# Kernel tuning notes

Hardware: AMD Instinct MI355X
Metric: run time of the kernel (lower is better)

The kernel has to match this reference:

```python
import jax, jax.numpy as jnp
import numpy as np

IN_CH = 8        # input_channels (includes time channel)
HID = 64         # hidden_channels
OUT = 1          # output_channels
MLP_W = 128      # CDEFunc hidden width
B, T = 4096, 166


def setup_inputs() -> dict:
    key = jax.random.key(0)
    ks = jax.random.split(key, 12)
    s = lambda fan_in: 1.0 / np.sqrt(fan_in)
    u0 = jax.random.normal(ks[0], (B, IN_CH - 1), dtype=jnp.float32)
    coeffs = jax.random.normal(ks[1], (B, T, IN_CH), dtype=jnp.float32)
    # CDEFunc params
    W1 = jax.random.uniform(ks[2], (HID, MLP_W), jnp.float32, -s(HID), s(HID))
    b1 = jax.random.uniform(ks[3], (MLP_W,), jnp.float32, -s(HID), s(HID))
    W2 = jax.random.uniform(ks[4], (MLP_W, IN_CH * HID), jnp.float32, -s(MLP_W), s(MLP_W))
    b2 = jax.random.uniform(ks[5], (IN_CH * HID,), jnp.float32, -s(MLP_W), s(MLP_W))
    # initial / readout linears
    Wi = jax.random.uniform(ks[6], (IN_CH - 1, HID), jnp.float32, -s(IN_CH - 1), s(IN_CH - 1))
    bi = jax.random.uniform(ks[7], (HID,), jnp.float32, -s(IN_CH - 1), s(IN_CH - 1))
    Wr = jax.random.uniform(ks[8], (HID, OUT), jnp.float32, -s(HID), s(HID))
    br = jax.random.uniform(ks[9], (OUT,), jnp.float32, -s(HID), s(HID))
    return {"u0": u0, "coeffs": coeffs, "W1": W1, "b1": b1, "W2": W2,
            "b2": b2, "Wi": Wi, "bi": bi, "Wr": Wr, "br": br}


def _cde_forward(u0, coeffs, W1, b1, W2, b2, Wi, bi, Wr, br):
    z0 = u0 @ Wi + bi                                  # [B, HID]
    # Linear interpolation on the knot grid t=0..T-1 with Euler steps of dt=1:
    # z_{k+1} = z_k + f(z_k) @ (X_{k+1} - X_k)
    dX = coeffs[:, 1:] - coeffs[:, :-1]                # [B, T-1, IN_CH]
    dX_t = jnp.swapaxes(dX, 0, 1)                      # [T-1, B, IN_CH]

    def step(z, dx):
        h = jax.nn.relu(z @ W1 + b1)                   # [B, MLP_W]
        f = jnp.tanh(h @ W2 + b2)                      # [B, IN_CH*HID]
        f = f.reshape(z.shape[0], HID, IN_CH)          # [B, HID, IN_CH]
        z_new = z + jnp.einsum('bhi,bi->bh', f, dx)
        return z_new, z_new

    _, zs = jax.lax.scan(step, z0, dX_t)               # [T-1, B, HID]
    z_all = jnp.concatenate([z0[None], zs], axis=0)    # [T, B, HID]
    z_all = jnp.swapaxes(z_all, 0, 1)                  # [B, T, HID]
    return z_all @ Wr + br                             # [B, T, OUT]


def reference(u0, coeffs, W1, b1, W2, b2, Wi, bi, Wr, br):
    return _cde_forward(u0, coeffs, W1, b1, W2, b2, Wi, bi, Wr, br)
```

## Files before the change

### kernel.cpp

```cpp
#include <hip/hip_runtime.h>


#define NBLK 256
#define NT   512
#define RB   16
#define T_LEN 166
#define IC   8
#define HID  64
#define MW   128
#define NF   512
#define ZSTR 65
#define DXSTR 12

typedef _Float16 half8 __attribute__((ext_vector_type(8)));
typedef _Float16 half4 __attribute__((ext_vector_type(4)));
typedef float    f32x4 __attribute__((ext_vector_type(4)));

__device__ __forceinline__ float fast_tanh(float x) {
    float e = __expf(2.0f * x);
    return 1.0f - 2.0f * __builtin_amdgcn_rcpf(e + 1.0f);
}

__global__ __launch_bounds__(NT, 2)
void cde_fused(const float* __restrict__ u0, const float* __restrict__ coeffs,
               const float* __restrict__ W1, const float* __restrict__ b1,
               const float* __restrict__ W2, const float* __restrict__ b2,
               const float* __restrict__ Wi, const float* __restrict__ bi,
               const float* __restrict__ Wr, const float* __restrict__ br,
               float* __restrict__ out)
{
    __shared__ __align__(16) unsigned char hh[RB * 256];
    __shared__ __align__(16) unsigned char hl[RB * 256];
    __shared__ __align__(16) unsigned char zh[RB * 128];
    __shared__ __align__(16) unsigned char zl[RB * 128];
    __shared__ float zbuf[RB * ZSTR];
    __shared__ __align__(16) float dxp[RB * DXSTR];

    const int tid  = threadIdx.x;
    const int lane = tid & 63;
    const int w    = tid >> 6;
    const int l15  = lane & 15;
    const int lq   = lane >> 4;
    const int swzr = (l15 & 7) << 4;
    const int b0   = blockIdx.x * RB;

    half8 w1h[2], w1l[2];
    #pragma unroll
    for (int kt = 0; kt < 2; ++kt) {
        const int krow = kt * 32 + lq * 8;
        const int ncol = w * 16 + l15;
        half8 vh, vl;
        #pragma unroll
        for (int j = 0; j < 8; ++j) {
            const float x = W1[(krow + j) * MW + ncol];
            const _Float16 hi = (_Float16)x;
            vh[j] = hi; vl[j] = (_Float16)(x - (float)hi);
        }
        w1h[kt] = vh; w1l[kt] = vl;
    }
    half8 w2h[16], w2l[16];
    #pragma unroll
    for (int q = 0; q < 4; ++q) {
        #pragma unroll
        for (int kt = 0; kt < 4; ++kt) {
            const int krow = kt * 32 + lq * 8;
            const int ncol = (w * 4 + q) * 16 + l15;
            half8 vh, vl;
            #pragma unroll
            for (int j = 0; j < 8; ++j) {
                const float x = W2[(krow + j) * NF + ncol];
                const _Float16 hi = (_Float16)x;
                vh[j] = hi; vl[j] = (_Float16)(x - (float)hi);
            }
            w2h[q * 4 + kt] = vh; w2l[q * 4 + kt] = vl;
        }
    }
    const f32x4 b1v = *(const f32x4*)(b1 + w * 16 + lq * 4);
    f32x4 b2v[4];
    #pragma unroll
    for (int q = 0; q < 4; ++q)
        b2v[q] = *(const f32x4*)(b2 + (w * 4 + q) * 16 + lq * 4);

    float wr0 = 0.f, wr1 = 0.f, wr2 = 0.f, wr3 = 0.f;
    const float brv = br[0];
    if (tid < 256) {
        const int seg = tid & 15;
        wr0 = Wr[seg * 4 + 0]; wr1 = Wr[seg * 4 + 1];
        wr2 = Wr[seg * 4 + 2]; wr3 = Wr[seg * 4 + 3];
    }

    #pragma unroll
    for (int s = 0; s < 2; ++s) {
        const int o = tid + NT * s;
        const int r = o >> 6, k = o & 63;
        float acc = bi[k];
        #pragma unroll
        for (int c = 0; c < 7; ++c) acc += u0[(b0 + r) * 7 + c] * Wi[c * HID + k];
        zbuf[r * ZSTR + k] = acc;
        const int byte = r * 128 + ((k * 2) ^ ((r & 7) << 4));
        const _Float16 hi = (_Float16)acc;
        *(_Float16*)(zh + byte) = hi;
        *(_Float16*)(zl + byte) = (_Float16)(acc - (float)hi);
    }
    __syncthreads();

    for (int t = 0; t < T_LEN; ++t) {
        if (tid < 256) {
            const int r = tid >> 4, seg = tid & 15;
            const float* zr = zbuf + r * ZSTR + seg * 4;
            float p = zr[0] * wr0 + zr[1] * wr1 + zr[2] * wr2 + zr[3] * wr3;
            p += __shfl_xor(p, 1, 64);
            p += __shfl_xor(p, 2, 64);
            p += __shfl_xor(p, 4, 64);
            p += __shfl_xor(p, 8, 64);
            if (seg == 0) out[(size_t)(b0 + r) * T_LEN + t] = p + brv;
        }
        if (t == T_LEN - 1) break;

        if (tid < 128) {
            const int r = tid >> 3, i = tid & 7;
            const float* cp = coeffs + ((size_t)(b0 + r) * T_LEN + t) * IC + i;
            dxp[r * DXSTR + i] = cp[IC] - cp[0];
        }

        f32x4 acc1 = {0.f, 0.f, 0.f, 0.f};
        #pragma unroll
        for (int kt = 0; kt < 2; ++kt) {
            const int off = l15 * 128 + ((kt * 64 + lq * 16) ^ swzr);
            const half8 zfh = *(const half8*)(zh + off);
            const half8 zfl = *(const half8*)(zl + off);
            acc1 = __builtin_amdgcn_mfma_f32_16x16x32_f16(w1h[kt], zfh, acc1, 0, 0, 0);
            acc1 = __builtin_amdgcn_mfma_f32_16x16x32_f16(w1l[kt], zfh, acc1, 0, 0, 0);
            acc1 = __builtin_amdgcn_mfma_f32_16x16x32_f16(w1h[kt], zfl, acc1, 0, 0, 0);
        }
        half4 ph, pl;
        #pragma unroll
        for (int r = 0; r < 4; ++r) {
            const float hv = fmaxf(acc1[r] + b1v[r], 0.0f);
            const _Float16 hi = (_Float16)hv;
            ph[r] = hi; pl[r] = (_Float16)(hv - (float)hi);
        }
        const int hoff = l15 * 256 + ((w * 32 + lq * 8) ^ swzr);
        *(half4*)(hh + hoff) = ph;
        *(half4*)(hl + hoff) = pl;
        __syncthreads();

        half8 bhf[4], blf[4];
        #pragma unroll
        for (int kt = 0; kt < 4; ++kt) {
            const int off = l15 * 256 + ((kt * 64 + lq * 16) ^ swzr);
            bhf[kt] = *(const half8*)(hh + off);
            blf[kt] = *(const half8*)(hl + off);
        }
        const f32x4 dxv = *(const f32x4*)(dxp + l15 * DXSTR + (lq & 1) * 4);
        #pragma unroll
        for (int q = 0; q < 4; ++q) {
            f32x4 acc = {0.f, 0.f, 0.f, 0.f};
            #pragma unroll
            for (int kt = 0; kt < 4; ++kt) {
                acc = __builtin_amdgcn_mfma_f32_16x16x32_f16(w2h[q * 4 + kt], bhf[kt], acc, 0, 0, 0);
                acc = __builtin_amdgcn_mfma_f32_16x16x32_f16(w2l[q * 4 + kt], bhf[kt], acc, 0, 0, 0);
                acc = __builtin_amdgcn_mfma_f32_16x16x32_f16(w2h[q * 4 + kt], blf[kt], acc, 0, 0, 0);
            }
            float s = 0.f;
            #pragma unroll
            for (int r = 0; r < 4; ++r) {
                const float f = fast_tanh(acc[r] + b2v[q][r]);
                s = fmaf(f, dxv[r], s);
            }
            s += __shfl_xor(s, 16, 64);
            if ((lq & 1) == 0) {
                const int kh = (w * 4 + q) * 2 + (lq >> 1);
                const float zn = zbuf[l15 * ZSTR + kh] + s;
                zbuf[l15 * ZSTR + kh] = zn;
                const _Float16 hi = (_Float16)zn;
                const int zoff = l15 * 128 + ((kh * 2) ^ swzr);
                *(_Float16*)(zh + zoff) = hi;
                *(_Float16*)(zl + zoff) = (_Float16)(zn - (float)hi);
            }
        }
        __syncthreads();
    }
}

extern "C" void kernel_launch(void* const* d_in, const int* in_sizes, int n_in,
                              void* d_out, int out_size, void* d_ws, size_t ws_size,
                              hipStream_t stream) {
    const float* u0     = (const float*)d_in[0];
    const float* coeffs = (const float*)d_in[1];
    const float* W1     = (const float*)d_in[2];
    const float* b1     = (const float*)d_in[3];
    const float* W2     = (const float*)d_in[4];
    const float* b2     = (const float*)d_in[5];
    const float* Wi     = (const float*)d_in[6];
    const float* bi     = (const float*)d_in[7];
    const float* Wr     = (const float*)d_in[8];
    const float* br     = (const float*)d_in[9];
    cde_fused<<<NBLK, NT, 0, stream>>>(u0, coeffs, W1, b1, W2, b2, Wi, bi, Wr, br,
                                       (float*)d_out);
}
```

Before: 320.2 us.

## Keep hidden state in registers, prefetch coeffs, use lgkm-only barriers

The fp32 hidden state now lives in per-wave registers (z8) instead of a shared zbuf, and updates use cross-lane shuffles. dX is computed in registers from a coefficient row prefetched one step ahead, so the per-step shared dxp staging is gone. The readout becomes per-wave partial dot products reduced by one wave, and __syncthreads is replaced by an LDS-only waitcnt plus s_barrier. Together these are meant to cut LDS traffic, global-load latency on the critical path and barrier cost in the serial time loop. The catch is that barrier correctness now depends on the inline asm waitcnt, and there is some extra register pressure.

```diff
diff --git a/kernel.cpp b/kernel.cpp
--- a/kernel.cpp
+++ b/kernel.cpp
@@ -5,12 +5,11 @@
 #define NT   512
 #define RB   16
 #define T_LEN 166
+#define NSTEP 165
 #define IC   8
 #define HID  64
 #define MW   128
 #define NF   512
-#define ZSTR 65
-#define DXSTR 12
 
 typedef _Float16 half8 __attribute__((ext_vector_type(8)));
 typedef _Float16 half4 __attribute__((ext_vector_type(4)));
@@ -19,6 +18,12 @@
 __device__ __forceinline__ float fast_tanh(float x) {
     float e = __expf(2.0f * x);
     return 1.0f - 2.0f * __builtin_amdgcn_rcpf(e + 1.0f);
+}
+
+__device__ __forceinline__ void bar_lgkm() {
+    asm volatile("s_waitcnt lgkmcnt(0)" ::: "memory");
+    __builtin_amdgcn_s_barrier();
+    __builtin_amdgcn_sched_barrier(0);
 }
 
 __global__ __launch_bounds__(NT, 2)
@@ -33,8 +38,7 @@
     __shared__ __align__(16) unsigned char hl[RB * 256];
     __shared__ __align__(16) unsigned char zh[RB * 128];
     __shared__ __align__(16) unsigned char zl[RB * 128];
-    __shared__ float zbuf[RB * ZSTR];
-    __shared__ __align__(16) float dxp[RB * DXSTR];
+    __shared__ float part[8][17];
 
     const int tid  = threadIdx.x;
     const int lane = tid & 63;
@@ -81,46 +85,54 @@
     for (int q = 0; q < 4; ++q)
         b2v[q] = *(const f32x4*)(b2 + (w * 4 + q) * 16 + lq * 4);
 
-    float wr0 = 0.f, wr1 = 0.f, wr2 = 0.f, wr3 = 0.f;
+    float wrs[8];
+    #pragma unroll
+    for (int j = 0; j < 8; ++j) wrs[j] = Wr[w * 8 + j];
     const float brv = br[0];
-    if (tid < 256) {
-        const int seg = tid & 15;
-        wr0 = Wr[seg * 4 + 0]; wr1 = Wr[seg * 4 + 1];
-        wr2 = Wr[seg * 4 + 2]; wr3 = Wr[seg * 4 + 3];
-    }
-
-    #pragma unroll
-    for (int s = 0; s < 2; ++s) {
-        const int o = tid + NT * s;
-        const int r = o >> 6, k = o & 63;
-        float acc = bi[k];
-        #pragma unroll
-        for (int c = 0; c < 7; ++c) acc += u0[(b0 + r) * 7 + c] * Wi[c * HID + k];
-        zbuf[r * ZSTR + k] = acc;
-        const int byte = r * 128 + ((k * 2) ^ ((r & 7) << 4));
-        const _Float16 hi = (_Float16)acc;
-        *(_Float16*)(zh + byte) = hi;
-        *(_Float16*)(zl + byte) = (_Float16)(acc - (float)hi);
-    }
+
+    float z8[8];
+    {
+        float uu[7];
+        const float* ur = u0 + (size_t)(b0 + l15) * 7;
+        #pragma unroll
+        for (int c = 0; c < 7; ++c) uu[c] = ur[c];
+        #pragma unroll
+        for (int j = 0; j < 8; ++j) {
+            float a = bi[w * 8 + j];
+            #pragma unroll
+            for (int c = 0; c < 7; ++c) a = fmaf(uu[c], Wi[c * HID + w * 8 + j], a);
+            z8[j] = a;
+        }
+    }
+    {
+        half8 hi8, lo8;
+        #pragma unroll
+        for (int j = 0; j < 8; ++j) {
+            const _Float16 hi = (_Float16)z8[j];
+            hi8[j] = hi; lo8[j] = (_Float16)(z8[j] - (float)hi);
+        }
+        if (lq == 0) {
+            const int zoff = l15 * 128 + ((w * 16) ^ swzr);
+            *(half8*)(zh + zoff) = hi8;
+            *(half8*)(zl + zoff) = lo8;
+            float rp = 0.f;
+            #pragma unroll
+            for (int j = 0; j < 8; ++j) rp = fmaf(z8[j], wrs[j], rp);
+            part[w][l15] = rp;
+        }
+    }
+    const float* cbase = coeffs + (size_t)(b0 + l15) * T_LEN * IC + (lq & 1) * 4;
+    f32x4 ccur = *(const f32x4*)(cbase);
     __syncthreads();
 
-    for (int t = 0; t < T_LEN; ++t) {
-        if (tid < 256) {
-            const int r = tid >> 4, seg = tid & 15;
-            const float* zr = zbuf + r * ZSTR + seg * 4;
-            float p = zr[0] * wr0 + zr[1] * wr1 + zr[2] * wr2 + zr[3] * wr3;
-            p += __shfl_xor(p, 1, 64);
-            p += __shfl_xor(p, 2, 64);
-            p += __shfl_xor(p, 4, 64);
-            p += __shfl_xor(p, 8, 64);
-            if (seg == 0) out[(size_t)(b0 + r) * T_LEN + t] = p + brv;
-        }
-        if (t == T_LEN - 1) break;
-
-        if (tid < 128) {
-            const int r = tid >> 3, i = tid & 7;
-            const float* cp = coeffs + ((size_t)(b0 + r) * T_LEN + t) * IC + i;
-            dxp[r * DXSTR + i] = cp[IC] - cp[0];
+    for (int t = 0; t < NSTEP; ++t) {
+        const f32x4 cnext = *(const f32x4*)(cbase + (size_t)(t + 1) * IC);
+
+        if (w == 7) {
+            float v = part[lq][l15] + part[lq + 4][l15];
+            v += __shfl_xor(v, 16, 64);
+            v += __shfl_xor(v, 32, 64);
+            if (lq == 0) out[(size_t)(b0 + l15) * T_LEN + t] = v + brv;
         }
 
         f32x4 acc1 = {0.f, 0.f, 0.f, 0.f};
@@ -143,7 +155,7 @@
         const int hoff = l15 * 256 + ((w * 32 + lq * 8) ^ swzr);
         *(half4*)(hh + hoff) = ph;
         *(half4*)(hl + hoff) = pl;
-        __syncthreads();
+        bar_lgkm();
 
         half8 bhf[4], blf[4];
         #pragma unroll
@@ -152,7 +164,7 @@
             bhf[kt] = *(const half8*)(hh + off);
             blf[kt] = *(const half8*)(hl + off);
         }
-        const f32x4 dxv = *(const f32x4*)(dxp + l15 * DXSTR + (lq & 1) * 4);
+        const f32x4 dxv = cnext - ccur;
         #pragma unroll
         for (int q = 0; q < 4; ++q) {
             f32x4 acc = {0.f, 0.f, 0.f, 0.f};
@@ -164,22 +176,39 @@
             }
             float s = 0.f;
             #pragma unroll
-            for (int r = 0; r < 4; ++r) {
-                const float f = fast_tanh(acc[r] + b2v[q][r]);
-                s = fmaf(f, dxv[r], s);
-            }
-            s += __shfl_xor(s, 16, 64);
-            if ((lq & 1) == 0) {
-                const int kh = (w * 4 + q) * 2 + (lq >> 1);
-                const float zn = zbuf[l15 * ZSTR + kh] + s;
-                zbuf[l15 * ZSTR + kh] = zn;
-                const _Float16 hi = (_Float16)zn;
-                const int zoff = l15 * 128 + ((kh * 2) ^ swzr);
-                *(_Float16*)(zh + zoff) = hi;
-                *(_Float16*)(zl + zoff) = (_Float16)(zn - (float)hi);
-            }
-        }
-        __syncthreads();
+            for (int r = 0; r < 4; ++r)
+                s = fmaf(fast_tanh(acc[r] + b2v[q][r]), dxv[r], s);
+            const float tt = s + __shfl_xor(s, 16, 64);
+            const float uu = __shfl_xor(tt, 32, 64);
+            z8[2 * q]     += tt;
+            z8[2 * q + 1] += uu;
+        }
+        {
+            half8 hi8, lo8;
+            #pragma unroll
+            for (int j = 0; j < 8; ++j) {
+                const _Float16 hi = (_Float16)z8[j];
+                hi8[j] = hi; lo8[j] = (_Float16)(z8[j] - (float)hi);
+            }
+            if (lq == 0) {
+                const int zoff = l15 * 128 + ((w * 16) ^ swzr);
+                *(half8*)(zh + zoff) = hi8;
+                *(half8*)(zl + zoff) = lo8;
+                float rp = 0.f;
+                #pragma unroll
+                for (int j = 0; j < 8; ++j) rp = fmaf(z8[j], wrs[j], rp);
+                part[w][l15] = rp;
+            }
+        }
+        ccur = cnext;
+        bar_lgkm();
+    }
+
+    if (w == 7) {
+        float v = part[lq][l15] + part[lq + 4][l15];
+        v += __shfl_xor(v, 16, 64);
+        v += __shfl_xor(v, 32, 64);
+        if (lq == 0) out[(size_t)(b0 + l15) * T_LEN + NSTEP] = v + brv;
     }
 }
 
```

Result: faster. 305.6 us (-4.6%).
